# Kernel optimization log

Hardware: AMD Instinct MI355X
Metric: run time of the kernel (lower is better)

## Reference

```python
import jax, jax.numpy as jnp
import numpy as np

N, E, F, H, O, B = 100000, 1200000, 64, 1024, 1, 256


def _gcn_conv(x, W, b, src, dst, ew, num_nodes):
    # PyG GCNConv: out_i = sum_{(s->i)} d_i^{-1/2} w_e d_s^{-1/2} (x_s W) + b
    deg = jax.ops.segment_sum(ew, dst, num_segments=num_nodes)
    dinv = jnp.where(deg > 0, jax.lax.rsqrt(jnp.maximum(deg, 1e-12)), 0.0)
    norm = dinv[src] * ew * dinv[dst]          # [E]
    h = x @ W                                   # [N, out]
    msg = h[src] * norm[:, None]                # gather + scale
    return jax.ops.segment_sum(msg, dst, num_segments=num_nodes) + b


def setup_inputs() -> dict:
    key = jax.random.key(0)
    ks = jax.random.split(key, 12)
    def lin(k, fan_in, fan_out):
        s = 1.0 / np.sqrt(fan_in)
        kw, kb = jax.random.split(k)
        return (jax.random.uniform(kw, (fan_in, fan_out), jnp.float32, -s, s),
                jax.random.uniform(kb, (fan_out,), jnp.float32, -s, s))
    W1, b1 = lin(ks[0], F, F)
    W2, b2 = lin(ks[1], F, 2 * F)
    W3, b3 = lin(ks[2], 2 * F, 4 * F)
    Wf1, bf1 = lin(ks[3], 5 * F, H)
    Wf2, bf2 = lin(ks[4], H, O)
    feature = jax.random.normal(ks[5], (N, F), jnp.float32)
    edge_index = jax.random.randint(ks[6], (2, E), 0, N, jnp.int32)
    weight = jax.random.uniform(ks[7], (E,), jnp.float32)
    protein_batch = jnp.sort(jax.random.randint(ks[8], (N,), 0, B, jnp.int32))
    return {"feature": feature, "edge_index": edge_index, "weight": weight,
            "protein_batch": protein_batch,
            "W1": W1, "b1": b1, "W2": W2, "b2": b2, "W3": W3, "b3": b3,
            "Wf1": Wf1, "bf1": bf1, "Wf2": Wf2, "bf2": bf2}


def reference(feature, edge_index, weight, protein_batch,
              W1, b1, W2, b2, W3, b3, Wf1, bf1, Wf2, bf2):
    num_nodes = feature.shape[0]
    # add self-loops with weight 1 (PyG default)
    loop = jnp.arange(num_nodes, dtype=edge_index.dtype)
    src = jnp.concatenate([edge_index[0], loop])
    dst = jnp.concatenate([edge_index[1], loop])
    ew = jnp.concatenate([weight, jnp.ones((num_nodes,), weight.dtype)])

    x = jax.nn.relu(_gcn_conv(feature, W1, b1, src, dst, ew, num_nodes))
    x = jax.nn.relu(_gcn_conv(x, W2, b2, src, dst, ew, num_nodes))
    x = jax.nn.relu(_gcn_conv(x, W3, b3, src, dst, ew, num_nodes))
    x = jnp.concatenate([x, feature], axis=1)   # [N, 5F]

    # global_mean_pool over graph ids
    sums = jax.ops.segment_sum(x, protein_batch, num_segments=B)
    cnts = jax.ops.segment_sum(jnp.ones((num_nodes,), x.dtype), protein_batch, num_segments=B)
    gc = sums / jnp.maximum(cnts, 1.0)[:, None]

    gc = jax.nn.relu(gc @ Wf1 + bf1)            # dropout is identity in eval
    return gc @ Wf2 + bf2
```

## Files before the change

### kernel.cpp

```cpp
#include <hip/hip_runtime.h>
#include <cstdio>
#include <cstdint>

typedef _Float16 f16x8 __attribute__((ext_vector_type(8)));
typedef float f32x4 __attribute__((ext_vector_type(4)));

__device__ inline unsigned short f2bf(float f) {
  unsigned u = __float_as_uint(f);
  u += 0x7fffu + ((u >> 16) & 1u);
  return (unsigned short)(u >> 16);
}
__device__ inline float bf2f(unsigned short h) {
  return __uint_as_float(((unsigned)h) << 16);
}
__device__ inline unsigned short f2h(float f) {
  union { _Float16 h; unsigned short u; } cv;
  cv.h = (_Float16)f;
  return cv.u;
}

#define EPB 8192


__global__ __launch_bounds__(256)
void k_prep0(float* __restrict__ psum,
             const float* __restrict__ feature, ushort* __restrict__ featb,
             const float* __restrict__ W1, ushort* __restrict__ w1h,
             const float* __restrict__ W2, ushort* __restrict__ w2h,
             const float* __restrict__ W3, ushort* __restrict__ w3h,
             const int* __restrict__ pb, int* __restrict__ gs,
             const int* __restrict__ dst, int* __restrict__ H,
             int* __restrict__ rs,
             int BC, int NF, int F, int D2, int D3,
             int N, int B, int NB, int E,
             int nB, int nC, int nD, int nG) {
  __shared__ int hist[512];
  int b = blockIdx.x;
  int t = threadIdx.x;
  if (b < nB) {
    int i = b * 256 + t;
    if (i < BC) psum[i] = 0.f;
  } else if (b < nB + nC) {
    int base = ((b - nB) * 256 + t) * 4;
    if (base < NF) {
      float4 v = *reinterpret_cast<const float4*>(feature + base);
      ushort4 h;
      h.x = f2bf(v.x); h.y = f2bf(v.y); h.z = f2bf(v.z); h.w = f2bf(v.w);
      *reinterpret_cast<ushort4*>(featb + base) = h;
    }
  } else if (b < nB + nC + nD) {
    int idx = (b - nB - nC) * 256 + t;
    int s1 = F * F, s2 = s1 + F * D2, s3 = s2 + D2 * D3;
    if (idx < s1) {
      int k = idx / F, n = idx - k * F;
      w1h[(size_t)n * F + k] = f2h(W1[idx]);
    } else if (idx < s2) {
      int i2 = idx - s1; int k = i2 / D2, n = i2 - k * D2;
      w2h[(size_t)n * F + k] = f2h(W2[i2]);
    } else if (idx < s3) {
      int i3 = idx - s2; int k = i3 / D3, n = i3 - k * D3;
      w3h[(size_t)n * D2 + k] = f2h(W3[i3]);
    }
  } else if (b < nB + nC + nD + nG) {
    int bb = (b - nB - nC - nD) * 256 + t;
    if (bb == 0) rs[N] = E;
    if (bb <= B) {
      int lo = 0, hi = N;
      while (lo < hi) {
        int mid = (lo + hi) >> 1;
        if (pb[mid] < bb) lo = mid + 1; else hi = mid;
      }
      gs[bb] = lo;
    }
  } else {
    const int bi = b - nB - nC - nD - nG;
    for (int i = t; i < NB; i += 256) hist[i] = 0;
    __syncthreads();
    const int base = bi * EPB + t;
#pragma unroll
    for (int j = 0; j < EPB / 256; j++) {
      int e = base + 256 * j;
      if (e < E) atomicAdd(&hist[dst[e] >> 8], 1);
    }
    __syncthreads();
    for (int i = t; i < NB; i += 256) H[(size_t)bi * NB + i] = hist[i];
  }
}

__global__ __launch_bounds__(256)
void k_bscan1(const int* __restrict__ H, int* __restrict__ S,
              int* __restrict__ bsum, int NB, int NBLK, int T) {
  __shared__ int sh[256];
  const int t = threadIdx.x;
  const int base = blockIdx.x * 1024;
  int v[4]; int s = 0;
#pragma unroll
  for (int j = 0; j < 4; j++) {
    int idx = base + t * 4 + j;
    if (idx < T) {
      int bin = idx / NBLK, bi = idx - bin * NBLK;
      v[j] = H[(size_t)bi * NB + bin];
    } else v[j] = 0;
    s += v[j];
  }
  sh[t] = s;
  __syncthreads();
  for (int off = 1; off < 256; off <<= 1) {
    int x = (t >= off) ? sh[t - off] : 0;
    __syncthreads();
    sh[t] += x;
    __syncthreads();
  }
  int run = sh[t] - s;
#pragma unroll
  for (int j = 0; j < 4; j++) {
    int idx = base + t * 4 + j;
    if (idx < T) S[idx] = run;
    run += v[j];
  }
  if (t == 255) bsum[blockIdx.x] = sh[255];
}

__device__ inline void build_prefix(const int* __restrict__ bsum, int nch,
                                    int* __restrict__ pre, int t) {
  for (int i = t; i < nch; i += 256) pre[i] = bsum[i];
  __syncthreads();
  if (t == 0) {
    int run = 0;
    for (int i = 0; i < nch; i++) { int v = pre[i]; pre[i] = run; run += v; }
  }
  __syncthreads();
}

__global__ __launch_bounds__(256)
void k_bscatter(const int* __restrict__ src, const int* __restrict__ dst,
                const float* __restrict__ ew, const int* __restrict__ S,
                const int* __restrict__ bsb,
                int2* __restrict__ ssw,
                int NB, int NBLK, int E, int nchT) {
  __shared__ int cnt[512];
  __shared__ int sbase[512];
  __shared__ int pre[512];
  const int t = threadIdx.x, bi = blockIdx.x;
  build_prefix(bsb, nchT, pre, t);
  for (int i = t; i < NB; i += 256) {
    cnt[i] = 0;
    int j = i * NBLK + bi;
    sbase[i] = S[j] + pre[j >> 10];
  }
  __syncthreads();
  const int base = bi * EPB + t;
#pragma unroll
  for (int j = 0; j < EPB / 256; j++) {
    int e = base + 256 * j;
    if (e < E) {
      int d = dst[e];
      int bin = d >> 8;
      int r = atomicAdd(&cnt[bin], 1);
      int pos = sbase[bin] + r;
      ssw[pos] = make_int2(src[e] | ((d & 255) << 24), __float_as_int(ew[e]));
    }
  }
}

__global__ __launch_bounds__(256)
void k_bprocA(const int2* __restrict__ ssw,
              const int* __restrict__ S, const int* __restrict__ bsb,
              int* __restrict__ cntN, float* __restrict__ wsumN,
              int NB, int NBLK, int N, int E, int nchT) {
  __shared__ int cnt[256];
  __shared__ float wsm[256];
  __shared__ int pre[512];
  const int t = threadIdx.x, bin = blockIdx.x;
  build_prefix(bsb, nchT, pre, t);
  cnt[t] = 0; wsm[t] = 0.f;
  __syncthreads();
  int j0 = bin * NBLK;
  const int start = S[j0] + pre[j0 >> 10];
  int end = E;
  if (bin + 1 < NB) { int j1 = (bin + 1) * NBLK; end = S[j1] + pre[j1 >> 10]; }
  for (int p = start + t; p < end; p += 256) {
    int2 sw = ssw[p];
    int ld = (unsigned)sw.x >> 24;
    atomicAdd(&cnt[ld], 1);
    atomicAdd(&wsm[ld], __int_as_float(sw.y));
  }
  __syncthreads();
  int n = bin * 256 + t;
  if (n < N) { cntN[n] = cnt[t]; wsumN[n] = wsm[t]; }
}

__global__ __launch_bounds__(256)
void k_scan1(const int* __restrict__ cntN, const float* __restrict__ wsumN,
             int* __restrict__ rs, int* __restrict__ bsum,
             float* __restrict__ dinv, float* __restrict__ sn, int N) {
  __shared__ int sh[256];
  const int t = threadIdx.x;
  const int base = blockIdx.x * 1024;
  int v[4]; int s = 0;
#pragma unroll
  for (int j = 0; j < 4; j++) {
    int idx = base + t * 4 + j;
    if (idx < N) {
      v[j] = cntN[idx];
      double deg = 1.0 + (double)wsumN[idx];
      float r = (float)(1.0 / sqrt(deg));
      dinv[idx] = r;
      sn[idx] = r * r;
    } else v[j] = 0;
    s += v[j];
  }
  sh[t] = s;
  __syncthreads();
  for (int off = 1; off < 256; off <<= 1) {
    int x = (t >= off) ? sh[t - off] : 0;
    __syncthreads();
    sh[t] += x;
    __syncthreads();
  }
  int run = sh[t] - s;
#pragma unroll
  for (int j = 0; j < 4; j++) {
    int idx = base + t * 4 + j;
    if (idx < N) rs[idx] = run;
    run += v[j];
  }
  if (t == 255) bsum[blockIdx.x] = sh[255];
}

__global__ __launch_bounds__(256)
void k_bprocB(const int2* __restrict__ ssw,
              const int* __restrict__ S, const int* __restrict__ bsb,
              int* __restrict__ rs, const int* __restrict__ bsumN,
              const float* __restrict__ dinv,
              int2* __restrict__ epack,
              int NB, int NBLK, int N, int E, int nchT, int nchN) {
  __shared__ int cnt[256];
  __shared__ float sdv[256];
  __shared__ int srs[256];
  __shared__ int preT[512];
  __shared__ int preN[128];
  const int t = threadIdx.x, bin = blockIdx.x;
  for (int i = t; i < nchT; i += 256) preT[i] = bsb[i];
  for (int i = t; i < nchN; i += 256) preN[i] = bsumN[i];
  __syncthreads();
  if (t == 0) {
    int run = 0;
    for (int i = 0; i < nchT; i++) { int v = preT[i]; preT[i] = run; run += v; }
    run = 0;
    for (int i = 0; i < nchN; i++) { int v = preN[i]; preN[i] = run; run += v; }
  }
  __syncthreads();
  cnt[t] = 0;
  int n = bin * 256 + t;
  sdv[t] = (n < N) ? dinv[n] : 0.f;
  int rabs = 0;
  if (n < N) {
    rabs = rs[n] + preN[n >> 10];
    rs[n] = rabs;
  }
  srs[t] = rabs;
  __syncthreads();
  int j0 = bin * NBLK;
  const int start = S[j0] + preT[j0 >> 10];
  int end = E;
  if (bin + 1 < NB) { int j1 = (bin + 1) * NBLK; end = S[j1] + preT[j1 >> 10]; }
  for (int p = start + t; p < end; p += 256) {
    int2 sw = ssw[p];
    int ld = (unsigned)sw.x >> 24;
    int sidx = sw.x & 0x00FFFFFF;
    int r = atomicAdd(&cnt[ld], 1);
    float w = dinv[sidx] * __int_as_float(sw.y) * sdv[ld];
    epack[srs[ld] + r] = make_int2(sidx, __float_as_int(w));
  }
}


__device__ inline void bf8_fma(const int4 v, float w, float* acc) {
  acc[0] = fmaf(__uint_as_float((unsigned)v.x << 16), w, acc[0]);
  acc[1] = fmaf(__uint_as_float((unsigned)v.x & 0xffff0000u), w, acc[1]);
  acc[2] = fmaf(__uint_as_float((unsigned)v.y << 16), w, acc[2]);
  acc[3] = fmaf(__uint_as_float((unsigned)v.y & 0xffff0000u), w, acc[3]);
  acc[4] = fmaf(__uint_as_float((unsigned)v.z << 16), w, acc[4]);
  acc[5] = fmaf(__uint_as_float((unsigned)v.z & 0xffff0000u), w, acc[5]);
  acc[6] = fmaf(__uint_as_float((unsigned)v.w << 16), w, acc[6]);
  acc[7] = fmaf(__uint_as_float((unsigned)v.w & 0xffff0000u), w, acc[7]);
}

template<int LOG2L>
__global__ __launch_bounds__(256)
void k_aggregate_b(const ushort* __restrict__ Xb, const int* __restrict__ rs,
                   const int2* __restrict__ epack, const float* __restrict__ sn,
                   ushort* __restrict__ AH, int N) {
  const int t = blockIdx.x * blockDim.x + threadIdx.x;
  const int row = t >> LOG2L;
  if (row >= N) return;
  const int L = 1 << LOG2L;
  const int D = L << 3;
  const int c = (t & (L - 1)) << 3;
  const ushort* __restrict__ Xc = Xb + c;

  float acc[8];
  {
    int4 v = *reinterpret_cast<const int4*>(Xc + (size_t)row * D);
    float s = sn[row];
    acc[0] = s * __uint_as_float((unsigned)v.x << 16);
    acc[1] = s * __uint_as_float((unsigned)v.x & 0xffff0000u);
    acc[2] = s * __uint_as_float((unsigned)v.y << 16);
    acc[3] = s * __uint_as_float((unsigned)v.y & 0xffff0000u);
    acc[4] = s * __uint_as_float((unsigned)v.z << 16);
    acc[5] = s * __uint_as_float((unsigned)v.z & 0xffff0000u);
    acc[6] = s * __uint_as_float((unsigned)v.w << 16);
    acc[7] = s * __uint_as_float((unsigned)v.w & 0xffff0000u);
  }
  const int p0 = rs[row], pe = rs[row + 1];
  int i = p0;
  if ((i & 1) && i < pe) {
    int2 e = epack[i];
    int4 v = *reinterpret_cast<const int4*>(Xc + (size_t)e.x * D);
    bf8_fma(v, __int_as_float(e.y), acc);
    i++;
  }
  for (; i + 8 <= pe; i += 8) {
    int4 ea = *reinterpret_cast<const int4*>(&epack[i]);
    int4 eb = *reinterpret_cast<const int4*>(&epack[i + 2]);
    int4 ec = *reinterpret_cast<const int4*>(&epack[i + 4]);
    int4 ed = *reinterpret_cast<const int4*>(&epack[i + 6]);
    int4 v0 = *reinterpret_cast<const int4*>(Xc + (size_t)ea.x * D);
    int4 v1 = *reinterpret_cast<const int4*>(Xc + (size_t)ea.z * D);
    int4 v2 = *reinterpret_cast<const int4*>(Xc + (size_t)eb.x * D);
    int4 v3 = *reinterpret_cast<const int4*>(Xc + (size_t)eb.z * D);
    int4 v4 = *reinterpret_cast<const int4*>(Xc + (size_t)ec.x * D);
    int4 v5 = *reinterpret_cast<const int4*>(Xc + (size_t)ec.z * D);
    int4 v6 = *reinterpret_cast<const int4*>(Xc + (size_t)ed.x * D);
    int4 v7 = *reinterpret_cast<const int4*>(Xc + (size_t)ed.z * D);
    bf8_fma(v0, __int_as_float(ea.y), acc);
    bf8_fma(v1, __int_as_float(ea.w), acc);
    bf8_fma(v2, __int_as_float(eb.y), acc);
    bf8_fma(v3, __int_as_float(eb.w), acc);
    bf8_fma(v4, __int_as_float(ec.y), acc);
    bf8_fma(v5, __int_as_float(ec.w), acc);
    bf8_fma(v6, __int_as_float(ed.y), acc);
    bf8_fma(v7, __int_as_float(ed.w), acc);
  }
  if (i + 4 <= pe) {
    int4 ea = *reinterpret_cast<const int4*>(&epack[i]);
    int4 eb = *reinterpret_cast<const int4*>(&epack[i + 2]);
    int4 v0 = *reinterpret_cast<const int4*>(Xc + (size_t)ea.x * D);
    int4 v1 = *reinterpret_cast<const int4*>(Xc + (size_t)ea.z * D);
    int4 v2 = *reinterpret_cast<const int4*>(Xc + (size_t)eb.x * D);
    int4 v3 = *reinterpret_cast<const int4*>(Xc + (size_t)eb.z * D);
    bf8_fma(v0, __int_as_float(ea.y), acc);
    bf8_fma(v1, __int_as_float(ea.w), acc);
    bf8_fma(v2, __int_as_float(eb.y), acc);
    bf8_fma(v3, __int_as_float(eb.w), acc);
    i += 4;
  }
  if (i + 2 <= pe) {
    int4 e2 = *reinterpret_cast<const int4*>(&epack[i]);
    int4 v0 = *reinterpret_cast<const int4*>(Xc + (size_t)e2.x * D);
    int4 v1 = *reinterpret_cast<const int4*>(Xc + (size_t)e2.z * D);
    bf8_fma(v0, __int_as_float(e2.y), acc);
    bf8_fma(v1, __int_as_float(e2.w), acc);
    i += 2;
  }
  if (i < pe) {
    int2 e = epack[i];
    int4 v = *reinterpret_cast<const int4*>(Xc + (size_t)e.x * D);
    bf8_fma(v, __int_as_float(e.y), acc);
  }
  ushort h[8];
#pragma unroll
  for (int j = 0; j < 8; j++) h[j] = f2h(acc[j]);
  size_t o = (size_t)row * D + c;
  *reinterpret_cast<ushort4*>(AH + o)     = make_ushort4(h[0], h[1], h[2], h[3]);
  *reinterpret_cast<ushort4*>(AH + o + 4) = make_ushort4(h[4], h[5], h[6], h[7]);
}


template<int KT, int TPB>
__global__ __launch_bounds__(256, 3)
void k_gemm_rb(const ushort* __restrict__ Ah, const ushort* __restrict__ Bh,
               const float* __restrict__ bias, ushort* __restrict__ Y,
               int N, int D) {
  constexpr int NT = 64;
  constexpr int NK = KT / 32;
  const int t = threadIdx.x;
  const int wave = t >> 6, lane = t & 63;
  const int quad = lane >> 4, l16 = lane & 15;
  const int n0 = blockIdx.x * NT;
  const int mbase = blockIdx.y * (TPB * 128);

  f16x8 bf[NK][4];
#pragma unroll
  for (int k0 = 0; k0 < NK; k0++)
#pragma unroll
    for (int ni = 0; ni < 4; ni++)
      bf[k0][ni] = *reinterpret_cast<const f16x8*>(
          Bh + (size_t)(n0 + ni * 16 + l16) * KT + k0 * 32 + quad * 8);

  float bv[4];
#pragma unroll
  for (int ni = 0; ni < 4; ni++) bv[ni] = bias[n0 + ni * 16 + l16];

#pragma unroll 1
  for (int tile = 0; tile < TPB; tile++) {
    const int rt = mbase + tile * 128 + wave * 32 + l16;
    if (mbase + tile * 128 >= N) break;
    int r0 = rt;      if (r0 >= N) r0 = N - 1;
    int r1 = rt + 16; if (r1 >= N) r1 = N - 1;
    const ushort* __restrict__ A0 = Ah + (size_t)r0 * KT + quad * 8;
    const ushort* __restrict__ A1 = Ah + (size_t)r1 * KT + quad * 8;

    f16x8 a0[NK], a1[NK];
#pragma unroll
    for (int k0 = 0; k0 < NK; k0++) {
      a0[k0] = *reinterpret_cast<const f16x8*>(A0 + k0 * 32);
      a1[k0] = *reinterpret_cast<const f16x8*>(A1 + k0 * 32);
    }

    f32x4 acc[2][4];
#pragma unroll
    for (int mi = 0; mi < 2; mi++)
#pragma unroll
      for (int ni = 0; ni < 4; ni++) acc[mi][ni] = (f32x4){0.f, 0.f, 0.f, 0.f};

#pragma unroll
    for (int k0 = 0; k0 < NK; k0++)
#pragma unroll
      for (int ni = 0; ni < 4; ni++) {
        acc[0][ni] = __builtin_amdgcn_mfma_f32_16x16x32_f16(a0[k0], bf[k0][ni], acc[0][ni], 0, 0, 0);
        acc[1][ni] = __builtin_amdgcn_mfma_f32_16x16x32_f16(a1[k0], bf[k0][ni], acc[1][ni], 0, 0, 0);
      }

    const int rb0 = mbase + tile * 128 + wave * 32 + quad * 4;
#pragma unroll
    for (int mi = 0; mi < 2; mi++) {
      int rb = rb0 + mi * 16;
#pragma unroll
      for (int ni = 0; ni < 4; ni++) {
        int col = n0 + ni * 16 + l16;
#pragma unroll
        for (int r = 0; r < 4; r++) {
          int row = rb + r;
          if (row < N)
            Y[(size_t)row * D + col] = f2bf(fmaxf(acc[mi][ni][r] + bv[ni], 0.f));
        }
      }
    }
  }
}


#define PSPLIT 8

__global__ void k_pool(const ushort* __restrict__ X3b, const float* __restrict__ feat,
                       const int* __restrict__ gs, float* __restrict__ psum,
                       int D3, int F) {
  const int c = threadIdx.x;
  const int C = D3 + F;
  const int b = blockIdx.y;
  const int sp = blockIdx.x;
  const int s0 = gs[b], e0 = gs[b + 1];
  const int len = e0 - s0;
  if (len <= 0) return;
  const int chunk = (len + PSPLIT - 1) / PSPLIT;
  const int s = s0 + sp * chunk;
  int e = s + chunk; if (e > e0) e = e0;
  if (s >= e) return;
  const int n = e - s;
  float a0 = 0.f, a1 = 0.f, a2 = 0.f, a3 = 0.f;
  float a4 = 0.f, a5 = 0.f, a6 = 0.f, a7 = 0.f;
  if (c < D3) {
    const ushort* p = X3b + (size_t)s * D3 + c;
    int i = 0;
    for (; i + 8 <= n; i += 8) {
      a0 += bf2f(p[0 * (size_t)D3]);
      a1 += bf2f(p[1 * (size_t)D3]);
      a2 += bf2f(p[2 * (size_t)D3]);
      a3 += bf2f(p[3 * (size_t)D3]);
      a4 += bf2f(p[4 * (size_t)D3]);
      a5 += bf2f(p[5 * (size_t)D3]);
      a6 += bf2f(p[6 * (size_t)D3]);
      a7 += bf2f(p[7 * (size_t)D3]);
      p += 8 * (size_t)D3;
    }
    for (; i < n; i++) { a0 += bf2f(*p); p += D3; }
  } else {
    const float* p = feat + (size_t)s * F + (c - D3);
    int i = 0;
    for (; i + 8 <= n; i += 8) {
      a0 += p[0 * (size_t)F];
      a1 += p[1 * (size_t)F];
      a2 += p[2 * (size_t)F];
      a3 += p[3 * (size_t)F];
      a4 += p[4 * (size_t)F];
      a5 += p[5 * (size_t)F];
      a6 += p[6 * (size_t)F];
      a7 += p[7 * (size_t)F];
      p += 8 * (size_t)F;
    }
    for (; i < n; i++) { a0 += *p; p += F; }
  }
  float tot = ((a0 + a1) + (a2 + a3)) + ((a4 + a5) + (a6 + a7));
  atomicAdd(&psum[(size_t)b * C + c], tot);
}


__global__ __launch_bounds__(256)
void k_fc1(const float* __restrict__ psum, const int* __restrict__ gs,
           const float* __restrict__ Wf1, const float* __restrict__ bf1,
           float* __restrict__ hidden, int C, int Hh) {
  const int b = blockIdx.y;
  __shared__ float gcs[384];
  float invc = 1.f / fmaxf((float)(gs[b + 1] - gs[b]), 1.f);
  for (int c = threadIdx.x; c < C; c += 256)
    gcs[c] = psum[(size_t)b * C + c] * invc;
  __syncthreads();
  const int j = blockIdx.x * 256 + threadIdx.x;
  if (j >= Hh) return;
  const float* w = Wf1 + j;
  float a0 = 0.f, a1 = 0.f, a2 = 0.f, a3 = 0.f;
  int c = 0;
  for (; c + 4 <= C; c += 4) {
    a0 = fmaf(gcs[c + 0], w[(size_t)(c + 0) * Hh], a0);
    a1 = fmaf(gcs[c + 1], w[(size_t)(c + 1) * Hh], a1);
    a2 = fmaf(gcs[c + 2], w[(size_t)(c + 2) * Hh], a2);
    a3 = fmaf(gcs[c + 3], w[(size_t)(c + 3) * Hh], a3);
  }
  for (; c < C; c++) a0 = fmaf(gcs[c], w[(size_t)c * Hh], a0);
  float r = ((a0 + a1) + (a2 + a3)) + bf1[j];
  hidden[(size_t)b * Hh + j] = fmaxf(r, 0.f);
}

__global__ void k_fc2(const float* __restrict__ hidden, const float* __restrict__ Wf2,
                      const float* __restrict__ bf2, float* __restrict__ out, int Hh) {
  int b = blockIdx.x;
  int lane = threadIdx.x;
  double s = 0.0;
  for (int j = lane; j < Hh; j += 64) s += (double)hidden[(size_t)b * Hh + j] * (double)Wf2[j];
#pragma unroll
  for (int off = 32; off > 0; off >>= 1) s += __shfl_down(s, off);
  if (lane == 0) out[b] = (float)s + bf2[0];
}


extern "C" void kernel_launch(void* const* d_in, const int* in_sizes, int n_in,
                              void* d_out, int out_size, void* d_ws, size_t ws_size,
                              hipStream_t stream) {
  const float* feature = (const float*)d_in[0];
  const int*   eidx    = (const int*)  d_in[1];
  const float* weight  = (const float*)d_in[2];
  const int*   pb      = (const int*)  d_in[3];
  const float* W1  = (const float*)d_in[4];
  const float* b1  = (const float*)d_in[5];
  const float* W2  = (const float*)d_in[6];
  const float* b2  = (const float*)d_in[7];
  const float* W3  = (const float*)d_in[8];
  const float* b3  = (const float*)d_in[9];
  const float* Wf1 = (const float*)d_in[10];
  const float* bf1 = (const float*)d_in[11];
  const float* Wf2 = (const float*)d_in[12];
  const float* bf2 = (const float*)d_in[13];

  const int F  = in_sizes[5];
  const int D2 = in_sizes[7];
  const int D3 = in_sizes[9];
  const int Hh = in_sizes[11];
  const int N  = in_sizes[0] / F;
  const int E  = in_sizes[1] / 2;
  const int B  = out_size;
  const int C  = D3 + F;

  const int* srcp = eidx;
  const int* dstp = eidx + E;

  const int NB   = (N + 255) / 256;
  const int NBLK = (E + EPB - 1) / EPB;
  const int T    = NB * NBLK;
  const int nchT = (T + 1023) / 1024;
  const int nchN = (N + 1023) / 1024;

  auto al = [](size_t x) { return (x + 255) & ~(size_t)255; };
  size_t off = 0;
  auto alloc = [&](size_t bytes) { size_t o = off; off += al(bytes); return o; };
  size_t o_H     = alloc((size_t)T * 4);
  size_t o_S     = alloc((size_t)T * 4);
  size_t o_bsb   = alloc((size_t)nchT * 4);
  size_t o_ssw   = alloc((size_t)E * 8);
  size_t o_cntN  = alloc((size_t)N * 4);
  size_t o_wsumN = alloc((size_t)N * 4);
  size_t o_dinv  = alloc((size_t)N * 4);
  size_t o_sn    = alloc((size_t)N * 4);
  size_t o_rs    = alloc((size_t)(N + 1) * 4);
  size_t o_bsum  = alloc((size_t)nchN * 4);
  size_t o_epack = alloc((size_t)E * 8);
  size_t o_featb = alloc((size_t)N * F  * 2);
  size_t o_x1b   = alloc((size_t)N * F  * 2);
  size_t o_x2b   = alloc((size_t)N * D2 * 2);
  size_t o_x3b   = alloc((size_t)N * D3 * 2);
  size_t o_aggh  = alloc((size_t)N * D2 * 2);
  size_t o_w1h   = alloc((size_t)F  * F  * 2);
  size_t o_w2h   = alloc((size_t)F  * D2 * 2);
  size_t o_w3h   = alloc((size_t)D2 * D3 * 2);
  size_t o_psum  = alloc((size_t)B * C * 4);
  size_t o_gs    = alloc((size_t)(B + 1) * 4);
  size_t o_hid   = alloc((size_t)B * Hh * 4);
  if (off > ws_size) {
    fprintf(stderr, "kernel_launch: workspace too small: need %zu, have %zu\n", off, ws_size);
    return;
  }

  char* ws = (char*)d_ws;
  int*    H     = (int*)  (ws + o_H);
  int*    S     = (int*)  (ws + o_S);
  int*    bsb   = (int*)  (ws + o_bsb);
  int2*   ssw   = (int2*) (ws + o_ssw);
  int*    cntN  = (int*)  (ws + o_cntN);
  float*  wsumN = (float*)(ws + o_wsumN);
  float*  dinv  = (float*)(ws + o_dinv);
  float*  sn    = (float*)(ws + o_sn);
  int*    rs    = (int*)  (ws + o_rs);
  int*    bsum  = (int*)  (ws + o_bsum);
  int2*   epack = (int2*) (ws + o_epack);
  ushort* featb = (ushort*)(ws + o_featb);
  ushort* x1b   = (ushort*)(ws + o_x1b);
  ushort* x2b   = (ushort*)(ws + o_x2b);
  ushort* x3b   = (ushort*)(ws + o_x3b);
  ushort* aggh  = (ushort*)(ws + o_aggh);
  ushort* w1h   = (ushort*)(ws + o_w1h);
  ushort* w2h   = (ushort*)(ws + o_w2h);
  ushort* w3h   = (ushort*)(ws + o_w3h);
  float*  psum  = (float*) (ws + o_psum);
  int*    gs    = (int*)  (ws + o_gs);
  float*  hid   = (float*)(ws + o_hid);
  float*  out   = (float*)d_out;

  const int BC = B * C, NF = N * F;
  const int nB = (BC + 255) / 256;
  const int nC = (NF / 4 + 255) / 256;
  const int nD = (F * F + F * D2 + D2 * D3 + 255) / 256;
  const int nG = (B + 1 + 255) / 256;
  k_prep0<<<nB + nC + nD + nG + NBLK, 256, 0, stream>>>(
      psum, feature, featb, W1, w1h, W2, w2h, W3, w3h,
      pb, gs, dstp, H, rs,
      BC, NF, F, D2, D3, N, B, NB, E, nB, nC, nD, nG);

  k_bscan1  <<<nchT, 256, 0, stream>>>(H, S, bsb, NB, NBLK, T);
  k_bscatter<<<NBLK, 256, 0, stream>>>(srcp, dstp, weight, S, bsb, ssw, NB, NBLK, E, nchT);
  k_bprocA  <<<NB, 256, 0, stream>>>(ssw, S, bsb, cntN, wsumN, NB, NBLK, N, E, nchT);
  k_scan1   <<<nchN, 256, 0, stream>>>(cntN, wsumN, rs, bsum, dinv, sn, N);
  k_bprocB  <<<NB, 256, 0, stream>>>(ssw, S, bsb, rs, bsum, dinv, epack, NB, NBLK, N, E, nchT, nchN);

  const int Mt = (N + 127) / 128;

  {
    int tot = N * (F / 8);
    k_aggregate_b<3><<<(tot + 255) / 256, 256, 0, stream>>>(featb, rs, epack, sn, aggh, N);
    dim3 g(1, Mt);
    k_gemm_rb<64, 1><<<g, 256, 0, stream>>>(aggh, w1h, b1, x1b, N, F);
  }
  {
    int tot = N * (F / 8);
    k_aggregate_b<3><<<(tot + 255) / 256, 256, 0, stream>>>(x1b, rs, epack, sn, aggh, N);
    dim3 g(2, (Mt + 1) / 2);
    k_gemm_rb<64, 2><<<g, 256, 0, stream>>>(aggh, w2h, b2, x2b, N, D2);
  }
  {
    int tot = N * (D2 / 8);
    k_aggregate_b<4><<<(tot + 255) / 256, 256, 0, stream>>>(x2b, rs, epack, sn, aggh, N);
    dim3 g(4, (Mt + 3) / 4);
    k_gemm_rb<128, 4><<<g, 256, 0, stream>>>(aggh, w3h, b3, x3b, N, D3);
  }

  {
    dim3 g(PSPLIT, B);
    k_pool<<<g, C, 0, stream>>>(x3b, feature, gs, psum, D3, F);
  }
  {
    dim3 g((Hh + 255) / 256, B);
    k_fc1<<<g, 256, 0, stream>>>(psum, gs, Wf1, bf1, hid, C, Hh);
  }
  k_fc2  <<<B, 64, 0, stream>>>(hid, Wf2, bf2, out, Hh);
}
```

Before: 384.3 us.

## Fuse layer-3 GEMM epilogue with global mean-pool accumulation via LDS slot sums

The third GCN layer's GEMM no longer writes the [N,256] bf16 activation. It applies bias and ReLU in registers and accumulates rows straight into per-graph pooled sums. Each block keeps 16 graph slots in shared memory, falls back to global atomics for graphs beyond those slots, then flushes nonzero slots to psum. This removes a large activation write and re-read, leaving the pool kernel to handle only the raw feature columns. The cost is many shared-memory atomics per element and possible global atomic contention.

```diff
diff --git a/kernel.cpp b/kernel.cpp
--- a/kernel.cpp
+++ b/kernel.cpp
@@ -452,11 +452,108 @@
 }
 
 
+#define NSLOT 16
+
+__global__ __launch_bounds__(256, 3)
+void k_gemm_pool(const ushort* __restrict__ Ah, const ushort* __restrict__ Bh,
+                 const float* __restrict__ bias, const int* __restrict__ pb,
+                 float* __restrict__ psum, int N, int C) {
+  constexpr int KT = 128, TPB = 4, NK = KT / 32;
+  __shared__ float sums[NSLOT][64];
+  const int t = threadIdx.x;
+  const int wave = t >> 6, lane = t & 63;
+  const int quad = lane >> 4, l16 = lane & 15;
+  const int n0 = blockIdx.x * 64;
+  const int mbase = blockIdx.y * (TPB * 128);
+
+  for (int i = t; i < NSLOT * 64; i += 256) ((float*)sums)[i] = 0.f;
+  const int g0 = pb[mbase < N ? mbase : N - 1];
+
+  f16x8 bf[NK][4];
+#pragma unroll
+  for (int k0 = 0; k0 < NK; k0++)
+#pragma unroll
+    for (int ni = 0; ni < 4; ni++)
+      bf[k0][ni] = *reinterpret_cast<const f16x8*>(
+          Bh + (size_t)(n0 + ni * 16 + l16) * KT + k0 * 32 + quad * 8);
+
+  float bv[4];
+#pragma unroll
+  for (int ni = 0; ni < 4; ni++) bv[ni] = bias[n0 + ni * 16 + l16];
+  __syncthreads();
+
+#pragma unroll 1
+  for (int tile = 0; tile < TPB; tile++) {
+    const int rt = mbase + tile * 128 + wave * 32 + l16;
+    if (mbase + tile * 128 >= N) break;
+    int r0 = rt;      if (r0 >= N) r0 = N - 1;
+    int r1 = rt + 16; if (r1 >= N) r1 = N - 1;
+    const ushort* __restrict__ A0 = Ah + (size_t)r0 * KT + quad * 8;
+    const ushort* __restrict__ A1 = Ah + (size_t)r1 * KT + quad * 8;
+
+    f16x8 a0[NK], a1[NK];
+#pragma unroll
+    for (int k0 = 0; k0 < NK; k0++) {
+      a0[k0] = *reinterpret_cast<const f16x8*>(A0 + k0 * 32);
+      a1[k0] = *reinterpret_cast<const f16x8*>(A1 + k0 * 32);
+    }
+
+    f32x4 acc[2][4];
+#pragma unroll
+    for (int mi = 0; mi < 2; mi++)
+#pragma unroll
+      for (int ni = 0; ni < 4; ni++) acc[mi][ni] = (f32x4){0.f, 0.f, 0.f, 0.f};
+
+#pragma unroll
+    for (int k0 = 0; k0 < NK; k0++)
+#pragma unroll
+      for (int ni = 0; ni < 4; ni++) {
+        acc[0][ni] = __builtin_amdgcn_mfma_f32_16x16x32_f16(a0[k0], bf[k0][ni], acc[0][ni], 0, 0, 0);
+        acc[1][ni] = __builtin_amdgcn_mfma_f32_16x16x32_f16(a1[k0], bf[k0][ni], acc[1][ni], 0, 0, 0);
+      }
+
+    const int rb0 = mbase + tile * 128 + wave * 32 + quad * 4;
+#pragma unroll
+    for (int mi = 0; mi < 2; mi++) {
+      const int rb = rb0 + mi * 16;
+      int gid[4]; int slot[4];
+#pragma unroll
+      for (int r = 0; r < 4; r++) {
+        int row = rb + r;
+        gid[r] = (row < N) ? pb[row] : -1;
+        slot[r] = gid[r] - g0;
+      }
+#pragma unroll
+      for (int ni = 0; ni < 4; ni++) {
+#pragma unroll
+        for (int r = 0; r < 4; r++) {
+          if (gid[r] >= 0) {
+            float v = fmaxf(acc[mi][ni][r] + bv[ni], 0.f);
+            if (slot[r] < NSLOT)
+              atomicAdd(&sums[slot[r]][ni * 16 + l16], v);
+            else
+              atomicAdd(&psum[(size_t)gid[r] * C + n0 + ni * 16 + l16], v);
+          }
+        }
+      }
+    }
+  }
+  __syncthreads();
+  for (int i = t; i < NSLOT * 64; i += 256) {
+    float v = ((float*)sums)[i];
+    if (v != 0.f) {
+      int slot = i >> 6, col = i & 63;
+      atomicAdd(&psum[(size_t)(g0 + slot) * C + n0 + col], v);
+    }
+  }
+}
+
+
 #define PSPLIT 8
 
-__global__ void k_pool(const ushort* __restrict__ X3b, const float* __restrict__ feat,
-                       const int* __restrict__ gs, float* __restrict__ psum,
-                       int D3, int F) {
+__global__ void k_poolf(const float* __restrict__ feat,
+                        const int* __restrict__ gs, float* __restrict__ psum,
+                        int D3, int F) {
   const int c = threadIdx.x;
   const int C = D3 + F;
   const int b = blockIdx.y;
@@ -471,39 +568,22 @@
   const int n = e - s;
   float a0 = 0.f, a1 = 0.f, a2 = 0.f, a3 = 0.f;
   float a4 = 0.f, a5 = 0.f, a6 = 0.f, a7 = 0.f;
-  if (c < D3) {
-    const ushort* p = X3b + (size_t)s * D3 + c;
-    int i = 0;
-    for (; i + 8 <= n; i += 8) {
-      a0 += bf2f(p[0 * (size_t)D3]);
-      a1 += bf2f(p[1 * (size_t)D3]);
-      a2 += bf2f(p[2 * (size_t)D3]);
-      a3 += bf2f(p[3 * (size_t)D3]);
-      a4 += bf2f(p[4 * (size_t)D3]);
-      a5 += bf2f(p[5 * (size_t)D3]);
-      a6 += bf2f(p[6 * (size_t)D3]);
-      a7 += bf2f(p[7 * (size_t)D3]);
-      p += 8 * (size_t)D3;
-    }
-    for (; i < n; i++) { a0 += bf2f(*p); p += D3; }
-  } else {
-    const float* p = feat + (size_t)s * F + (c - D3);
-    int i = 0;
-    for (; i + 8 <= n; i += 8) {
-      a0 += p[0 * (size_t)F];
-      a1 += p[1 * (size_t)F];
-      a2 += p[2 * (size_t)F];
-      a3 += p[3 * (size_t)F];
-      a4 += p[4 * (size_t)F];
-      a5 += p[5 * (size_t)F];
-      a6 += p[6 * (size_t)F];
-      a7 += p[7 * (size_t)F];
-      p += 8 * (size_t)F;
-    }
-    for (; i < n; i++) { a0 += *p; p += F; }
-  }
+  const float* p = feat + (size_t)s * F + c;
+  int i = 0;
+  for (; i + 8 <= n; i += 8) {
+    a0 += p[0 * (size_t)F];
+    a1 += p[1 * (size_t)F];
+    a2 += p[2 * (size_t)F];
+    a3 += p[3 * (size_t)F];
+    a4 += p[4 * (size_t)F];
+    a5 += p[5 * (size_t)F];
+    a6 += p[6 * (size_t)F];
+    a7 += p[7 * (size_t)F];
+    p += 8 * (size_t)F;
+  }
+  for (; i < n; i++) { a0 += *p; p += F; }
   float tot = ((a0 + a1) + (a2 + a3)) + ((a4 + a5) + (a6 + a7));
-  atomicAdd(&psum[(size_t)b * C + c], tot);
+  atomicAdd(&psum[(size_t)b * C + D3 + c], tot);
 }
 
 
@@ -598,7 +678,6 @@
   size_t o_featb = alloc((size_t)N * F  * 2);
   size_t o_x1b   = alloc((size_t)N * F  * 2);
   size_t o_x2b   = alloc((size_t)N * D2 * 2);
-  size_t o_x3b   = alloc((size_t)N * D3 * 2);
   size_t o_aggh  = alloc((size_t)N * D2 * 2);
   size_t o_w1h   = alloc((size_t)F  * F  * 2);
   size_t o_w2h   = alloc((size_t)F  * D2 * 2);
@@ -626,7 +705,6 @@
   ushort* featb = (ushort*)(ws + o_featb);
   ushort* x1b   = (ushort*)(ws + o_x1b);
   ushort* x2b   = (ushort*)(ws + o_x2b);
-  ushort* x3b   = (ushort*)(ws + o_x3b);
   ushort* aggh  = (ushort*)(ws + o_aggh);
   ushort* w1h   = (ushort*)(ws + o_w1h);
   ushort* w2h   = (ushort*)(ws + o_w2h);
@@ -670,12 +748,12 @@
     int tot = N * (D2 / 8);
     k_aggregate_b<4><<<(tot + 255) / 256, 256, 0, stream>>>(x2b, rs, epack, sn, aggh, N);
     dim3 g(4, (Mt + 3) / 4);
-    k_gemm_rb<128, 4><<<g, 256, 0, stream>>>(aggh, w3h, b3, x3b, N, D3);
+    k_gemm_pool<<<g, 256, 0, stream>>>(aggh, w3h, b3, pb, psum, N, C);
   }
 
   {
     dim3 g(PSPLIT, B);
-    k_pool<<<g, C, 0, stream>>>(x3b, feature, gs, psum, D3, F);
+    k_poolf<<<g, F, 0, stream>>>(feature, gs, psum, D3, F);
   }
   {
     dim3 g((Hh + 255) / 256, B);
```

New measurement: 508.9 us. 32.4% more time.
